# Kernel tuning notes

Measured on AMD Instinct MI355X. Metric: run time of the kernel, lower is better.

The kernel has to match this reference:

```python
import jax, jax.numpy as jnp
import numpy as np


def _gcn_conv(x, W, b, src, dst, dinv):
    # PyG GCNConv: linear transform, then symmetric-normalized aggregation, then bias
    n = x.shape[0]
    h = x @ W  # [N, out]
    norm = (dinv[src] * dinv[dst])[:, None]  # [E, 1]
    msg = h[src] * norm  # gather + scale, [E, out]
    out = jax.ops.segment_sum(msg, dst, num_segments=n)  # scatter-add
    return out + b


def setup_inputs() -> dict:
    key = jax.random.key(0)
    k1, k2, k3, k4 = jax.random.split(key, 4)
    N, E, F_IN, F_HID, F_OUT = 50000, 800000, 512, 256, 64
    x = jax.random.normal(k1, (N, F_IN), dtype=jnp.float32)
    edge_index = jax.random.randint(k2, (2, E), 0, N, dtype=jnp.int64)
    # Glorot-ish init for weights
    W1 = jax.random.normal(k3, (F_IN, F_HID), dtype=jnp.float32) * (1.0 / np.sqrt(F_IN))
    b1 = jnp.zeros((F_HID,), dtype=jnp.float32)
    W2 = jax.random.normal(k4, (F_HID, F_OUT), dtype=jnp.float32) * (1.0 / np.sqrt(F_HID))
    b2 = jnp.zeros((F_OUT,), dtype=jnp.float32)
    return {"x": x, "edge_index": edge_index, "W1": W1, "b1": b1, "W2": W2, "b2": b2}


def reference(x, edge_index, W1, b1, W2, b2):
    n = x.shape[0]
    # Add self loops (GCNConv default)
    loop = jnp.arange(n, dtype=edge_index.dtype)
    src = jnp.concatenate([edge_index[0], loop])
    dst = jnp.concatenate([edge_index[1], loop])
    # Symmetric normalization D^{-1/2} (A+I) D^{-1/2}
    deg = jax.ops.segment_sum(jnp.ones_like(dst, dtype=x.dtype), dst, num_segments=n)
    dinv = jnp.where(deg > 0, jax.lax.rsqrt(deg), 0.0)
    h = _gcn_conv(x, W1, b1, src, dst, dinv)
    h = jax.nn.relu(h)
    # Dropout(p=0.5) is identity in eval mode (deterministic reference)
    h = _gcn_conv(h, W2, b2, src, dst, dinv)
    return jax.nn.log_softmax(h, axis=1)
```

## Files before the change

### kernel.cpp

```cpp
#include <hip/hip_runtime.h>
#include <math.h>

#define F_IN  512
#define F_HID 256
#define F_OUT 64

typedef __attribute__((ext_vector_type(8))) short bf16x8;
typedef __attribute__((ext_vector_type(4))) short bf16x4;
typedef __attribute__((ext_vector_type(4))) float f32x4;

#define GLOBAL_AS __attribute__((address_space(1)))
#define LDS_AS    __attribute__((address_space(3)))

__device__ __forceinline__ void gload_lds16(const ushort* g, ushort* l) {
    __builtin_amdgcn_global_load_lds((const GLOBAL_AS uint32_t*)g,
                                     (LDS_AS uint32_t*)l, 16, 0, 0);
}

__device__ __forceinline__ ushort f2bf(float f) {
    union { float f; uint32_t u; } v; v.f = f;
    uint32_t r = (v.u + 0x7FFFu + ((v.u >> 16) & 1u)) >> 16;
    return (ushort)r;
}

__device__ __forceinline__ float bf2f(ushort u) {
    union { uint32_t u; float f; } v; v.u = ((uint32_t)u) << 16;
    return v.f;
}

__global__ void k_deg(const int* __restrict__ dst, int* __restrict__ deg, int E) {
    int e = blockIdx.x * 256 + threadIdx.x;
    if (e < E) atomicAdd(&deg[dst[e]], 1);
}

__global__ void k_scan1(const int* __restrict__ deg, int* __restrict__ offs,
                        int* __restrict__ bsums, float* __restrict__ dinv, int N) {
    __shared__ int s[256];
    int tid = threadIdx.x;
    int i = blockIdx.x * 256 + tid;
    int v = (i < N) ? deg[i] : 0;
    if (i < N) dinv[i] = rsqrtf((float)(v + 1));
    s[tid] = v; __syncthreads();
    for (int d = 1; d < 256; d <<= 1) {
        int t = (tid >= d) ? s[tid - d] : 0;
        __syncthreads();
        s[tid] += t;
        __syncthreads();
    }
    if (i < N) offs[i] = s[tid] - v;
    if (tid == 255) bsums[blockIdx.x] = s[255];
}

__global__ void k_scan2(int* __restrict__ bsums, int n) {
    __shared__ int s[256];
    int tid = threadIdx.x;
    int v = (tid < n) ? bsums[tid] : 0;
    s[tid] = v; __syncthreads();
    for (int d = 1; d < 256; d <<= 1) {
        int t = (tid >= d) ? s[tid - d] : 0;
        __syncthreads();
        s[tid] += t;
        __syncthreads();
    }
    if (tid < n) bsums[tid] = s[tid] - v;
}

__global__ void k_scan3(int* __restrict__ offs, const int* __restrict__ bsums,
                        int* __restrict__ cursor, int2* __restrict__ jw, int N, int E) {
    int i = blockIdx.x * 256 + threadIdx.x;
    if (i < N) {
        int o = offs[i] + bsums[i >> 8];
        offs[i] = o;
        cursor[i] = o;
    }
    if (i == 0) offs[N] = E;
    if (i < 16) jw[E + i] = make_int2(0, 0);
}

__global__ void k_fill(const int* __restrict__ src, const int* __restrict__ dst,
                       int* __restrict__ cursor, int2* __restrict__ jw,
                       const float* __restrict__ dinv, int E) {
    int e = blockIdx.x * 256 + threadIdx.x;
    if (e < E) {
        int s = src[e];
        int pos = atomicAdd(&cursor[dst[e]], 1);
        jw[pos] = make_int2(s, __float_as_int(dinv[s]));
    }
}

__global__ void k_tcast2(const float* __restrict__ W1, ushort* __restrict__ w1t,
                         const float* __restrict__ W2, ushort* __restrict__ w2t) {
    int idx = blockIdx.x * 256 + threadIdx.x;
    const int n1 = F_IN * F_HID;
    if (idx < n1) {
        int n = idx / F_IN, k = idx - n * F_IN;
        w1t[idx] = f2bf(W1[(size_t)k * F_HID + n]);
    } else {
        int t = idx - n1;
        if (t < F_HID * F_OUT) {
            int n = t / F_HID, k = t - n * F_HID;
            w2t[t] = f2bf(W2[(size_t)k * F_OUT + n]);
        }
    }
}

__global__ __launch_bounds__(256) void k_gemm1(
        const float* __restrict__ A, const ushort* __restrict__ Bt,
        ushort* __restrict__ C, int M) {
    constexpr int K = F_IN, Nc = F_HID, BM = 128, BN = 128;
    constexpr int ASTR = 36;
    __shared__ ushort As[BM * ASTR];
    __shared__ ushort Bs[BN * 32];
    const int tid  = threadIdx.x;
    const int wave = tid >> 6, lane = tid & 63;
    const int wr = wave & 1, wc = wave >> 1;
    const int brow = blockIdx.y * BM, bcol = blockIdx.x * BN;

    f32x4 acc[4][4];
    #pragma unroll
    for (int m = 0; m < 4; ++m)
        #pragma unroll
        for (int n = 0; n < 4; ++n) acc[m][n] = (f32x4){0.f, 0.f, 0.f, 0.f};

    const int arow = tid >> 1;
    const int akh  = (tid & 1) * 16;
    int agrow = brow + arow; if (agrow >= M) agrow = M - 1;
    const float4* aptr = (const float4*)&A[(size_t)agrow * K];
    const int srow = tid >> 2;
    const int scol = (tid & 3) * 8;

    const int kq  = (lane >> 4) * 8;
    const int rA0 = wr * 64 + (lane & 15);
    const int rB0 = wc * 64 + (lane & 15);

    float4 v0 = aptr[akh / 4 + 0], v1 = aptr[akh / 4 + 1],
           v2 = aptr[akh / 4 + 2], v3 = aptr[akh / 4 + 3];

    for (int k0 = 0; k0 < K; k0 += 32) {
        bf16x8 a0, a1_;
        a0[0] = (short)f2bf(v0.x); a0[1] = (short)f2bf(v0.y);
        a0[2] = (short)f2bf(v0.z); a0[3] = (short)f2bf(v0.w);
        a0[4] = (short)f2bf(v1.x); a0[5] = (short)f2bf(v1.y);
        a0[6] = (short)f2bf(v1.z); a0[7] = (short)f2bf(v1.w);
        a1_[0] = (short)f2bf(v2.x); a1_[1] = (short)f2bf(v2.y);
        a1_[2] = (short)f2bf(v2.z); a1_[3] = (short)f2bf(v2.w);
        a1_[4] = (short)f2bf(v3.x); a1_[5] = (short)f2bf(v3.y);
        a1_[6] = (short)f2bf(v3.z); a1_[7] = (short)f2bf(v3.w);
        *(bf16x8*)&As[arow * ASTR + akh]     = a0;
        *(bf16x8*)&As[arow * ASTR + akh + 8] = a1_;
        #pragma unroll
        for (int l = 0; l < 2; ++l)
            gload_lds16(&Bt[(size_t)(bcol + l * 64 + srow) * K + k0 + scol],
                        &Bs[l * 2048 + wave * 512]);
        __syncthreads();
        if (k0 + 32 < K) {
            int b = (k0 + 32 + akh) / 4;
            v0 = aptr[b]; v1 = aptr[b + 1]; v2 = aptr[b + 2]; v3 = aptr[b + 3];
        }
        bf16x8 af[4], bfr[4];
        #pragma unroll
        for (int m = 0; m < 4; ++m)
            af[m] = *(const bf16x8*)&As[(rA0 + m * 16) * ASTR + kq];
        #pragma unroll
        for (int n = 0; n < 4; ++n)
            bfr[n] = *(const bf16x8*)&Bs[(rB0 + n * 16) * 32 + kq];
        #pragma unroll
        for (int m = 0; m < 4; ++m)
            #pragma unroll
            for (int n = 0; n < 4; ++n)
                acc[m][n] = __builtin_amdgcn_mfma_f32_16x16x32_bf16(af[m], bfr[n], acc[m][n], 0, 0, 0);
        __syncthreads();
    }

    const int crow0 = brow + wr * 64 + (lane >> 4) * 4;
    const int ccol0 = bcol + wc * 64 + (lane & 15);
    #pragma unroll
    for (int m = 0; m < 4; ++m)
        #pragma unroll
        for (int n = 0; n < 4; ++n)
            #pragma unroll
            for (int j = 0; j < 4; ++j) {
                int row = crow0 + m * 16 + j;
                if (row < M) C[(size_t)row * Nc + ccol0 + n * 16] = f2bf(acc[m][n][j]);
            }
}

template<int WR, int WC, int MR, int NR>
__global__ __launch_bounds__(256) void k_gemm_bf16(
        const ushort* __restrict__ A, const ushort* __restrict__ Bt,
        ushort* __restrict__ C, int M, int K, int Nc) {
    constexpr int BM = WR * MR * 16;
    constexpr int BN = WC * NR * 16;
    __shared__ ushort As[BM * 32];
    __shared__ ushort Bs[BN * 32];
    const int tid  = threadIdx.x;
    const int wave = tid >> 6, lane = tid & 63;
    const int wr = wave % WR, wc = wave / WR;
    const int brow = blockIdx.y * BM, bcol = blockIdx.x * BN;

    f32x4 acc[MR][NR];
    #pragma unroll
    for (int m = 0; m < MR; ++m)
        #pragma unroll
        for (int n = 0; n < NR; ++n) acc[m][n] = (f32x4){0.f, 0.f, 0.f, 0.f};

    const int srow = tid >> 2;
    const int scol = (tid & 3) * 8;
    const int kq  = (lane >> 4) * 8;
    const int rA0 = wr * MR * 16 + (lane & 15);
    const int rB0 = wc * NR * 16 + (lane & 15);

    for (int k0 = 0; k0 < K; k0 += 32) {
        #pragma unroll
        for (int l = 0; l < BM / 64; ++l) {
            int row = brow + l * 64 + srow;
            if (row >= M) row = M - 1;
            gload_lds16(&A[(size_t)row * K + k0 + scol], &As[l * 2048 + wave * 512]);
        }
        #pragma unroll
        for (int l = 0; l < BN / 64; ++l) {
            int row = bcol + l * 64 + srow;
            gload_lds16(&Bt[(size_t)row * K + k0 + scol], &Bs[l * 2048 + wave * 512]);
        }
        __syncthreads();
        bf16x8 af[MR], bfr[NR];
        #pragma unroll
        for (int m = 0; m < MR; ++m)
            af[m] = *(const bf16x8*)&As[(rA0 + m * 16) * 32 + kq];
        #pragma unroll
        for (int n = 0; n < NR; ++n)
            bfr[n] = *(const bf16x8*)&Bs[(rB0 + n * 16) * 32 + kq];
        #pragma unroll
        for (int m = 0; m < MR; ++m)
            #pragma unroll
            for (int n = 0; n < NR; ++n)
                acc[m][n] = __builtin_amdgcn_mfma_f32_16x16x32_bf16(af[m], bfr[n], acc[m][n], 0, 0, 0);
        __syncthreads();
    }

    const int crow0 = brow + wr * MR * 16 + (lane >> 4) * 4;
    const int ccol0 = bcol + wc * NR * 16 + (lane & 15);
    #pragma unroll
    for (int m = 0; m < MR; ++m)
        #pragma unroll
        for (int n = 0; n < NR; ++n)
            #pragma unroll
            for (int j = 0; j < 4; ++j) {
                int row = crow0 + m * 16 + j;
                if (row < M) C[(size_t)row * Nc + ccol0 + n * 16] = f2bf(acc[m][n][j]);
            }
}

__global__ __launch_bounds__(256) void k_agg1(
        const ushort* __restrict__ h, const int2* __restrict__ jw,
        const int* __restrict__ offs, const float* __restrict__ dinv,
        const float* __restrict__ bias, ushort* __restrict__ outm, int N) {
    int wave = threadIdx.x >> 6, lane = threadIdx.x & 63;
    int i = blockIdx.x * 4 + wave;
    if (i >= N) return;
    int g = lane & 31;
    int p = lane >> 5;
    float di = dinv[i];
    float acc[8];
    {
        bf16x8 hv = *(const bf16x8*)&h[(size_t)i * F_HID + g * 8];
        float w = (p == 0) ? di * di : 0.f;
        #pragma unroll
        for (int k = 0; k < 8; ++k) acc[k] = bf2f((ushort)hv[k]) * w;
    }
    int s = offs[i], e = offs[i + 1];
    for (int u = s; u < e; u += 12) {
        int2 a[6];
        #pragma unroll
        for (int q = 0; q < 6; ++q) a[q] = jw[u + 2 * q + p];
        bf16x8 hv[6];
        #pragma unroll
        for (int q = 0; q < 6; ++q)
            hv[q] = *(const bf16x8*)&h[(size_t)a[q].x * F_HID + g * 8];
        #pragma unroll
        for (int q = 0; q < 6; ++q) {
            float ww = (u + 2 * q + p < e) ? __int_as_float(a[q].y) * di : 0.f;
            #pragma unroll
            for (int k = 0; k < 8; ++k) acc[k] += bf2f((ushort)hv[q][k]) * ww;
        }
    }
    #pragma unroll
    for (int k = 0; k < 8; ++k) acc[k] += __shfl_xor(acc[k], 32, 64);
    if (p == 0) {
        float4 b0 = *(const float4*)&bias[g * 8];
        float4 b1 = *(const float4*)&bias[g * 8 + 4];
        bf16x8 o;
        o[0] = (short)f2bf(fmaxf(acc[0] + b0.x, 0.f));
        o[1] = (short)f2bf(fmaxf(acc[1] + b0.y, 0.f));
        o[2] = (short)f2bf(fmaxf(acc[2] + b0.z, 0.f));
        o[3] = (short)f2bf(fmaxf(acc[3] + b0.w, 0.f));
        o[4] = (short)f2bf(fmaxf(acc[4] + b1.x, 0.f));
        o[5] = (short)f2bf(fmaxf(acc[5] + b1.y, 0.f));
        o[6] = (short)f2bf(fmaxf(acc[6] + b1.z, 0.f));
        o[7] = (short)f2bf(fmaxf(acc[7] + b1.w, 0.f));
        *(bf16x8*)&outm[(size_t)i * F_HID + g * 8] = o;
    }
}

__global__ __launch_bounds__(256) void k_agg2(
        const ushort* __restrict__ h, const int2* __restrict__ jw,
        const int* __restrict__ offs, const float* __restrict__ dinv,
        const float* __restrict__ bias, float* __restrict__ outm, int N) {
    int wave = threadIdx.x >> 6, lane = threadIdx.x & 63;
    int i = blockIdx.x * 4 + wave;
    if (i >= N) return;
    float di = dinv[i];
    float acc = bf2f(h[(size_t)i * F_OUT + lane]) * di * di;
    int s = offs[i], e = offs[i + 1];
    for (int u = s; u < e; u += 8) {
        int2 a[8];
        #pragma unroll
        for (int q = 0; q < 8; ++q) a[q] = jw[u + q];
        float hv[8];
        #pragma unroll
        for (int q = 0; q < 8; ++q)
            hv[q] = bf2f(h[(size_t)a[q].x * F_OUT + lane]);
        #pragma unroll
        for (int q = 0; q < 8; ++q) {
            float ww = (u + q < e) ? __int_as_float(a[q].y) * di : 0.f;
            acc += hv[q] * ww;
        }
    }
    acc += bias[lane];
    float m = acc;
    #pragma unroll
    for (int o = 32; o >= 1; o >>= 1) m = fmaxf(m, __shfl_xor(m, o, 64));
    float ex = expf(acc - m);
    float ssum = ex;
    #pragma unroll
    for (int o = 32; o >= 1; o >>= 1) ssum += __shfl_xor(ssum, o, 64);
    outm[(size_t)i * F_OUT + lane] = acc - m - logf(ssum);
}

extern "C" void kernel_launch(void* const* d_in, const int* in_sizes, int n_in,
                              void* d_out, int out_size, void* d_ws, size_t ws_size,
                              hipStream_t stream) {
    const float* x  = (const float*)d_in[0];
    const int*   ei = (const int*)d_in[1];
    const float* W1 = (const float*)d_in[2];
    const float* b1 = (const float*)d_in[3];
    const float* W2 = (const float*)d_in[4];
    const float* b2 = (const float*)d_in[5];
    float* out = (float*)d_out;

    int N = in_sizes[0] / F_IN;
    int E = in_sizes[1] / 2;
    const int* src = ei;
    const int* dst = ei + E;

    ushort* w1t = (ushort*)d_ws;
    ushort* w2t = w1t + F_HID * F_IN;
    ushort* h1  = w2t + F_OUT * F_HID;
    ushort* a1  = h1 + (size_t)N * F_HID;
    int*    deg = (int*)(a1 + (size_t)N * F_HID);
    float*  dinv = (float*)(deg + N);
    int*    offs = (int*)(dinv + N);
    int*    cursor = offs + N + 1;
    int*    bsums  = cursor + N;
    int2*   jw = (int2*)(((uintptr_t)(bsums + 256) + 7) & ~(uintptr_t)7);
    ushort* h2 = h1;

    int nch = (N + 255) / 256;

    hipMemsetAsync(deg, 0, sizeof(int) * N, stream);
    k_deg <<<(E + 255) / 256, 256, 0, stream>>>(dst, deg, E);
    k_scan1<<<nch, 256, 0, stream>>>(deg, offs, bsums, dinv, N);
    k_scan2<<<1, 256, 0, stream>>>(bsums, nch);
    k_scan3<<<nch, 256, 0, stream>>>(offs, bsums, cursor, jw, N, E);
    k_fill<<<(E + 255) / 256, 256, 0, stream>>>(src, dst, cursor, jw, dinv, E);

    int ntc = F_IN * F_HID + F_HID * F_OUT;
    k_tcast2<<<(ntc + 255) / 256, 256, 0, stream>>>(W1, w1t, W2, w2t);

    k_gemm1<<<dim3(F_HID / 128, (N + 127) / 128), 256, 0, stream>>>(x, w1t, h1, N);
    k_agg1<<<(N + 3) / 4, 256, 0, stream>>>(h1, jw, offs, dinv, b1, a1, N);

    k_gemm_bf16<4, 1, 2, 4><<<dim3(1, (N + 127) / 128), 256, 0, stream>>>(
        a1, w2t, h2, N, F_HID, F_OUT);
    k_agg2<<<(N + 3) / 4, 256, 0, stream>>>(h2, jw, offs, dinv, b2, out, N);
}
```

Before: 262.1 us.

## Double-buffer LDS in first GEMM and XOR-swizzle B tile layout

```diff
diff --git a/kernel.cpp b/kernel.cpp
--- a/kernel.cpp
+++ b/kernel.cpp
@@ -107,10 +107,10 @@
 __global__ __launch_bounds__(256) void k_gemm1(
         const float* __restrict__ A, const ushort* __restrict__ Bt,
         ushort* __restrict__ C, int M) {
-    constexpr int K = F_IN, Nc = F_HID, BM = 128, BN = 128;
+    constexpr int K = F_IN, Nc = F_HID, BM = 128, BN = 128, NT = K / 32;
     constexpr int ASTR = 36;
-    __shared__ ushort As[BM * ASTR];
-    __shared__ ushort Bs[BN * 32];
+    __shared__ ushort As[2][BM * ASTR];
+    __shared__ ushort Bs[2][BN * 32];
     const int tid  = threadIdx.x;
     const int wave = tid >> 6, lane = tid & 63;
     const int wr = wave & 1, wc = wave >> 1;
@@ -125,51 +125,76 @@
     const int arow = tid >> 1;
     const int akh  = (tid & 1) * 16;
     int agrow = brow + arow; if (agrow >= M) agrow = M - 1;
-    const float4* aptr = (const float4*)&A[(size_t)agrow * K];
+    const float4* ap = (const float4*)&A[(size_t)agrow * K + akh];
     const int srow = tid >> 2;
-    const int scol = (tid & 3) * 8;
-
-    const int kq  = (lane >> 4) * 8;
+    const int csrc = (lane & 3) ^ ((lane >> 3) & 3);
+    const ushort* bp0 = &Bt[(size_t)(bcol + srow) * K + csrc * 8];
+    const ushort* bp1 = &Bt[(size_t)(bcol + 64 + srow) * K + csrc * 8];
+
+    const int kqA = (lane >> 4) * 8;
+    const int kqB = ((lane >> 4) ^ ((lane >> 1) & 3)) * 8;
     const int rA0 = wr * 64 + (lane & 15);
     const int rB0 = wc * 64 + (lane & 15);
 
-    float4 v0 = aptr[akh / 4 + 0], v1 = aptr[akh / 4 + 1],
-           v2 = aptr[akh / 4 + 2], v3 = aptr[akh / 4 + 3];
-
-    for (int k0 = 0; k0 < K; k0 += 32) {
-        bf16x8 a0, a1_;
-        a0[0] = (short)f2bf(v0.x); a0[1] = (short)f2bf(v0.y);
-        a0[2] = (short)f2bf(v0.z); a0[3] = (short)f2bf(v0.w);
-        a0[4] = (short)f2bf(v1.x); a0[5] = (short)f2bf(v1.y);
-        a0[6] = (short)f2bf(v1.z); a0[7] = (short)f2bf(v1.w);
-        a1_[0] = (short)f2bf(v2.x); a1_[1] = (short)f2bf(v2.y);
-        a1_[2] = (short)f2bf(v2.z); a1_[3] = (short)f2bf(v2.w);
-        a1_[4] = (short)f2bf(v3.x); a1_[5] = (short)f2bf(v3.y);
-        a1_[6] = (short)f2bf(v3.z); a1_[7] = (short)f2bf(v3.w);
-        *(bf16x8*)&As[arow * ASTR + akh]     = a0;
-        *(bf16x8*)&As[arow * ASTR + akh + 8] = a1_;
-        #pragma unroll
-        for (int l = 0; l < 2; ++l)
-            gload_lds16(&Bt[(size_t)(bcol + l * 64 + srow) * K + k0 + scol],
-                        &Bs[l * 2048 + wave * 512]);
-        __syncthreads();
-        if (k0 + 32 < K) {
-            int b = (k0 + 32 + akh) / 4;
-            v0 = aptr[b]; v1 = aptr[b + 1]; v2 = aptr[b + 2]; v3 = aptr[b + 3];
+    float4 rA[2][4];
+
+    #pragma unroll
+    for (int q = 0; q < 4; ++q) rA[0][q] = ap[q];
+    gload_lds16(bp0, &Bs[0][wave * 512]);
+    gload_lds16(bp1, &Bs[0][2048 + wave * 512]);
+    {
+        bf16x8 c0, c1;
+        c0[0] = (short)f2bf(rA[0][0].x); c0[1] = (short)f2bf(rA[0][0].y);
+        c0[2] = (short)f2bf(rA[0][0].z); c0[3] = (short)f2bf(rA[0][0].w);
+        c0[4] = (short)f2bf(rA[0][1].x); c0[5] = (short)f2bf(rA[0][1].y);
+        c0[6] = (short)f2bf(rA[0][1].z); c0[7] = (short)f2bf(rA[0][1].w);
+        c1[0] = (short)f2bf(rA[0][2].x); c1[1] = (short)f2bf(rA[0][2].y);
+        c1[2] = (short)f2bf(rA[0][2].z); c1[3] = (short)f2bf(rA[0][2].w);
+        c1[4] = (short)f2bf(rA[0][3].x); c1[5] = (short)f2bf(rA[0][3].y);
+        c1[6] = (short)f2bf(rA[0][3].z); c1[7] = (short)f2bf(rA[0][3].w);
+        *(bf16x8*)&As[0][arow * ASTR + akh]     = c0;
+        *(bf16x8*)&As[0][arow * ASTR + akh + 8] = c1;
+    }
+    #pragma unroll
+    for (int q = 0; q < 4; ++q) rA[1][q] = ap[8 + q];
+    __syncthreads();
+
+    #pragma unroll
+    for (int t = 0; t < NT; ++t) {
+        const int b = t & 1;
+        if (t + 1 < NT) {
+            gload_lds16(bp0 + (t + 1) * 32, &Bs[b ^ 1][wave * 512]);
+            gload_lds16(bp1 + (t + 1) * 32, &Bs[b ^ 1][2048 + wave * 512]);
+            const float4* r = rA[(t + 1) & 1];
+            bf16x8 c0, c1;
+            c0[0] = (short)f2bf(r[0].x); c0[1] = (short)f2bf(r[0].y);
+            c0[2] = (short)f2bf(r[0].z); c0[3] = (short)f2bf(r[0].w);
+            c0[4] = (short)f2bf(r[1].x); c0[5] = (short)f2bf(r[1].y);
+            c0[6] = (short)f2bf(r[1].z); c0[7] = (short)f2bf(r[1].w);
+            c1[0] = (short)f2bf(r[2].x); c1[1] = (short)f2bf(r[2].y);
+            c1[2] = (short)f2bf(r[2].z); c1[3] = (short)f2bf(r[2].w);
+            c1[4] = (short)f2bf(r[3].x); c1[5] = (short)f2bf(r[3].y);
+            c1[6] = (short)f2bf(r[3].z); c1[7] = (short)f2bf(r[3].w);
+            *(bf16x8*)&As[b ^ 1][arow * ASTR + akh]     = c0;
+            *(bf16x8*)&As[b ^ 1][arow * ASTR + akh + 8] = c1;
+        }
+        if (t + 2 < NT) {
+            #pragma unroll
+            for (int q = 0; q < 4; ++q) rA[t & 1][q] = ap[(t + 2) * 8 + q];
         }
         bf16x8 af[4], bfr[4];
         #pragma unroll
         for (int m = 0; m < 4; ++m)
-            af[m] = *(const bf16x8*)&As[(rA0 + m * 16) * ASTR + kq];
+            af[m] = *(const bf16x8*)&As[b][(rA0 + m * 16) * ASTR + kqA];
         #pragma unroll
         for (int n = 0; n < 4; ++n)
-            bfr[n] = *(const bf16x8*)&Bs[(rB0 + n * 16) * 32 + kq];
+            bfr[n] = *(const bf16x8*)&Bs[b][(rB0 + n * 16) * 32 + kqB];
         #pragma unroll
         for (int m = 0; m < 4; ++m)
             #pragma unroll
             for (int n = 0; n < 4; ++n)
                 acc[m][n] = __builtin_amdgcn_mfma_f32_16x16x32_bf16(af[m], bfr[n], acc[m][n], 0, 0, 0);
-        __syncthreads();
+        if (t + 1 < NT) __syncthreads();
     }
 
     const int crow0 = brow + wr * 64 + (lane >> 4) * 4;
```

Result: no change. 260.4 us (-0.6%).
